# Performance work log

Hardware: AMD Instinct MI355X
Metric: run time of the kernel (lower is better)

Reference implementation:

```python
import jax, jax.numpy as jnp
import numpy as np

EPS = 1e-8  # torch.nn.CosineSimilarity default eps


def setup_inputs() -> dict:
    key = jax.random.key(0)
    k1, k2 = jax.random.split(key)
    action_set = jax.random.normal(k1, (1_000_000, 64), dtype=jnp.float32)
    pred_action = jax.random.normal(k2, (32, 4, 64), dtype=jnp.float32)
    return {"pred_action": pred_action, "action_set": action_set}


def reference(pred_action, action_set):
    # pred_action: [B, T, D] (a 2-D [B, D] input would be unsqueezed to T=1)
    # action_set:  [N, D]
    if pred_action.ndim == 2:
        pred_action = pred_action[:, None, :]
    # torch CosineSimilarity: x1.x2 / max(||x1|| * ||x2||, eps)
    dot = jnp.einsum('nd,btd->nbt', action_set, pred_action)        # [N, B, T]
    na = jnp.linalg.norm(action_set, axis=-1)                       # [N]
    nb = jnp.linalg.norm(pred_action, axis=-1)                      # [B, T]
    sims = dot / jnp.maximum(na[:, None, None] * nb[None, :, :], EPS)
    amax = jnp.argmax(sims, axis=0)                                  # [B, T]
    return action_set[amax]                                          # [B, T, D]
```

## Files before the change

kernel.cpp:

```cpp
#include <hip/hip_runtime.h>
#include <hip/hip_bf16.h>
#include <math.h>

#define D        64
#define NQ       128
#define TS       64
#define ASTRIDE  72
#define MARGIN   0.025f
#define CAP      128

typedef __attribute__((ext_vector_type(8))) short  short8;
typedef __attribute__((ext_vector_type(4))) short  short4v;
typedef __attribute__((ext_vector_type(4))) float  f32x4;

__device__ inline unsigned ordf(float f) {
    unsigned u = __float_as_uint(f);
    return (u & 0x80000000u) ? ~u : (u | 0x80000000u);
}

__device__ inline short bf16bits(float f) {
    __hip_bfloat16 h = __float2bfloat16(f);
    return *(short*)&h;
}

__device__ inline float sq4(f32x4 a) {
    float s = 0.f;
    s = fmaf(a.x, a.x, s); s = fmaf(a.y, a.y, s);
    s = fmaf(a.z, a.z, s); s = fmaf(a.w, a.w, s);
    return s;
}

__device__ inline float sq16(f32x4 a, f32x4 b, f32x4 c, f32x4 d) {
    return sq4(a) + sq4(b) + sq4(c) + sq4(d);
}

__device__ inline short8 cvt8(f32x4 a, f32x4 b, float s) {
    short8 r;
    r[0] = bf16bits(a.x * s); r[1] = bf16bits(a.y * s);
    r[2] = bf16bits(a.z * s); r[3] = bf16bits(a.w * s);
    r[4] = bf16bits(b.x * s); r[5] = bf16bits(b.y * s);
    r[6] = bf16bits(b.z * s); r[7] = bf16bits(b.w * s);
    return r;
}

__device__ inline short4v cvt4(f32x4 a, float s) {
    short4v r;
    r[0] = bf16bits(a.x * s); r[1] = bf16bits(a.y * s);
    r[2] = bf16bits(a.z * s); r[3] = bf16bits(a.w * s);
    return r;
}

__global__ __launch_bounds__(256, 3)
void k1_score(const float* __restrict__ pred,
              const float* __restrict__ acts,
              float* __restrict__ tmax,
              int ntiles)
{
    __shared__ unsigned short As[2][TS * ASTRIDE];

    const int tid  = threadIdx.x;
    const int lane = tid & 63;
    const int wv   = tid >> 6;
    const int quad = lane >> 4;
    const int l15  = lane & 15;

    short8 bf[2][2];
#pragma unroll
    for (int nt = 0; nt < 2; ++nt) {
        const int q = (wv * 2 + nt) * 16 + l15;
        const float* P = pred + q * D + quad * 8;
        f32x4 v0 = *(const f32x4*)(P);
        f32x4 v1 = *(const f32x4*)(P + 4);
        f32x4 v2 = *(const f32x4*)(P + 32);
        f32x4 v3 = *(const f32x4*)(P + 36);
        float nb2 = sq16(v0, v1, v2, v3);
        nb2 += __shfl_xor(nb2, 16);
        nb2 += __shfl_xor(nb2, 32);
        const float rnb = 1.0f / sqrtf(nb2);
        bf[nt][0] = cvt8(v0, v1, rnb);
        bf[nt][1] = cvt8(v2, v3, rnb);
    }

    int tile = blockIdx.x;
    if (tile >= ntiles) return;

    {
        const f32x4* src = (const f32x4*)(acts + (size_t)tile * (TS * D));
        f32x4 v[4];
#pragma unroll
        for (int i = 0; i < 4; ++i) v[i] = src[tid + i * 256];
#pragma unroll
        for (int i = 0; i < 4; ++i) {
            const int c   = tid + i * 256;
            const int row = c >> 4, col = c & 15;
            float s = sq4(v[i]);
            s += __shfl_xor(s, 1); s += __shfl_xor(s, 2);
            s += __shfl_xor(s, 4); s += __shfl_xor(s, 8);
            *(short4v*)&As[0][row * ASTRIDE + col * 4] = cvt4(v[i], 1.0f / sqrtf(s));
        }
    }
    __syncthreads();

    int p = 0;
    while (true) {
        const int tn = tile + gridDim.x;
        const bool have_next = tn < ntiles;

        f32x4 v[4];
        if (have_next) {
            const f32x4* src = (const f32x4*)(acts + (size_t)tn * (TS * D));
#pragma unroll
            for (int i = 0; i < 4; ++i) v[i] = src[tid + i * 256];
        }

        short8 af[4][2];
#pragma unroll
        for (int mt = 0; mt < 4; ++mt)
#pragma unroll
            for (int ks = 0; ks < 2; ++ks)
                af[mt][ks] = *(const short8*)
                    &As[p][(mt * 16 + l15) * ASTRIDE + ks * 32 + quad * 8];

        f32x4 acc[2][4];
#pragma unroll
        for (int nt = 0; nt < 2; ++nt)
#pragma unroll
            for (int mt = 0; mt < 4; ++mt) acc[nt][mt] = (f32x4){0.f, 0.f, 0.f, 0.f};
#pragma unroll
        for (int ks = 0; ks < 2; ++ks)
#pragma unroll
            for (int nt = 0; nt < 2; ++nt)
#pragma unroll
                for (int mt = 0; mt < 4; ++mt)
                    acc[nt][mt] = __builtin_amdgcn_mfma_f32_16x16x32_bf16(
                        af[mt][ks], bf[nt][ks], acc[nt][mt], 0, 0, 0);

#pragma unroll
        for (int nt = 0; nt < 2; ++nt) {
            float m = -3.0e38f;
#pragma unroll
            for (int mt = 0; mt < 4; ++mt)
                m = fmaxf(m, fmaxf(fmaxf(acc[nt][mt].x, acc[nt][mt].y),
                                   fmaxf(acc[nt][mt].z, acc[nt][mt].w)));
            m = fmaxf(m, __shfl_xor(m, 16));
            m = fmaxf(m, __shfl_xor(m, 32));
            if (quad == 0) {
                const int q = (wv * 2 + nt) * 16 + l15;
                tmax[(size_t)q * ntiles + tile] = m;
            }
        }

        if (!have_next) break;

#pragma unroll
        for (int i = 0; i < 4; ++i) {
            const int c   = tid + i * 256;
            const int row = c >> 4, col = c & 15;
            float s = sq4(v[i]);
            s += __shfl_xor(s, 1); s += __shfl_xor(s, 2);
            s += __shfl_xor(s, 4); s += __shfl_xor(s, 8);
            *(short4v*)&As[p ^ 1][row * ASTRIDE + col * 4] = cvt4(v[i], 1.0f / sqrtf(s));
        }
        __syncthreads();
        p ^= 1;
        tile = tn;
    }
}

__global__ __launch_bounds__(256, 2)
void k2_rescore(const float* __restrict__ pred,
                const float* __restrict__ acts,
                const float* __restrict__ tmax,
                float* __restrict__ out,
                int ntiles)
{
    __shared__ float wmax[4];
    __shared__ int   cnt;
    __shared__ int   list[CAP];

    const int q   = blockIdx.x;
    const int tid = threadIdx.x;
    const float* row = tmax + (size_t)q * ntiles;

    if (tid == 0) cnt = 0;
    float m = -3.0e38f;
    for (int t = tid; t < ntiles; t += 256) m = fmaxf(m, row[t]);
#pragma unroll
    for (int off = 1; off < 64; off <<= 1) m = fmaxf(m, __shfl_xor(m, off));
    if ((tid & 63) == 0) wmax[tid >> 6] = m;
    __syncthreads();
    m = fmaxf(fmaxf(wmax[0], wmax[1]), fmaxf(wmax[2], wmax[3]));
    const float thr = m - MARGIN;

    for (int t = tid; t < ntiles; t += 256) {
        if (row[t] >= thr) {
            int i = atomicAdd(&cnt, 1);
            if (i < CAP) list[i] = t;
        }
    }
    __syncthreads();
    const int n = min(cnt, CAP);

    if (tid < 64) {
        const f32x4* P = (const f32x4*)(pred + q * D);
        unsigned long long best = 0ull;
        for (int i = 0; i < n; ++i) {
            const int r = list[i] * TS + tid;
            const f32x4* A = (const f32x4*)(acts + (size_t)r * D);
            float dot = 0.f, na2 = 0.f;
#pragma unroll
            for (int c = 0; c < 16; ++c) {
                f32x4 a = A[c];
                f32x4 pq = P[c];
                dot = fmaf(a.x, pq.x, dot); na2 = fmaf(a.x, a.x, na2);
                dot = fmaf(a.y, pq.y, dot); na2 = fmaf(a.y, a.y, na2);
                dot = fmaf(a.z, pq.z, dot); na2 = fmaf(a.z, a.z, na2);
                dot = fmaf(a.w, pq.w, dot); na2 = fmaf(a.w, a.w, na2);
            }
            float sim = dot * (1.0f / sqrtf(na2));
            unsigned long long key =
                ((unsigned long long)ordf(sim) << 32) | (unsigned)(~r);
#pragma unroll
            for (int off = 1; off < 64; off <<= 1) {
                unsigned long long o = __shfl_xor(key, off);
                if (o > key) key = o;
            }
            if (key > best) best = key;
        }
        const unsigned idx = ~(unsigned)(best & 0xffffffffull);
        out[q * D + tid] = acts[(size_t)idx * D + tid];
    }
}

extern "C" void kernel_launch(void* const* d_in, const int* in_sizes, int n_in,
                              void* d_out, int out_size, void* d_ws, size_t ws_size,
                              hipStream_t stream)
{
    const float* pred = (const float*)d_in[0];
    const float* acts = (const float*)d_in[1];
    long n0 = in_sizes[0], n1 = in_sizes[1];
    if (n0 > n1) {
        const float* t = pred; pred = acts; acts = t;
        long tt = n0; n0 = n1; n1 = tt;
    }
    const int N      = (int)(n1 / D);
    const int ntiles = N / TS;

    float* tmax = (float*)d_ws;
    float* out  = (float*)d_out;

    k1_score<<<dim3(768), dim3(256), 0, stream>>>(pred, acts, tmax, ntiles);
    k2_rescore<<<dim3(NQ), dim3(256), 0, stream>>>(pred, acts, tmax, out, ntiles);
}
```

Measured before the change: 382.4 us.

## Assign contiguous tile chunks per block and coalesce tmax writes via LDS

Each block of the scoring kernel now processes a contiguous chunk of 21 tiles instead of grid-strided tiles. Per-tile maxima are buffered in shared memory and written to tmax in row-contiguous runs at the end, replacing the scattered per-tile stores. The rescoring kernel spreads candidate tiles across all four waves and reduces the best key once at the end, instead of running one wave with a shuffle reduction per candidate. The extra shared buffer lowers occupancy headroom, and the grid size now depends on ntiles.

```diff
diff --git a/kernel.cpp b/kernel.cpp
--- a/kernel.cpp
+++ b/kernel.cpp
@@ -8,6 +8,7 @@
 #define ASTRIDE  72
 #define MARGIN   0.025f
 #define CAP      128
+#define CHUNK    21
 
 typedef __attribute__((ext_vector_type(8))) short  short8;
 typedef __attribute__((ext_vector_type(4))) short  short4v;
@@ -57,12 +58,17 @@
               int ntiles)
 {
     __shared__ unsigned short As[2][TS * ASTRIDE];
+    __shared__ float tbuf[NQ * CHUNK];
 
     const int tid  = threadIdx.x;
     const int lane = tid & 63;
     const int wv   = tid >> 6;
     const int quad = lane >> 4;
     const int l15  = lane & 15;
+
+    const int tile0 = blockIdx.x * CHUNK;
+    if (tile0 >= ntiles) return;
+    const int cn = min(CHUNK, ntiles - tile0);
 
     short8 bf[2][2];
 #pragma unroll
@@ -81,11 +87,8 @@
         bf[nt][1] = cvt8(v2, v3, rnb);
     }
 
-    int tile = blockIdx.x;
-    if (tile >= ntiles) return;
-
     {
-        const f32x4* src = (const f32x4*)(acts + (size_t)tile * (TS * D));
+        const f32x4* src = (const f32x4*)(acts + (size_t)tile0 * (TS * D));
         f32x4 v[4];
 #pragma unroll
         for (int i = 0; i < 4; ++i) v[i] = src[tid + i * 256];
@@ -101,14 +104,15 @@
     }
     __syncthreads();
 
-    int p = 0;
+    int ti = 0;
+    int p  = 0;
     while (true) {
-        const int tn = tile + gridDim.x;
-        const bool have_next = tn < ntiles;
+        const bool have_next = (ti + 1) < cn;
 
         f32x4 v[4];
         if (have_next) {
-            const f32x4* src = (const f32x4*)(acts + (size_t)tn * (TS * D));
+            const f32x4* src =
+                (const f32x4*)(acts + (size_t)(tile0 + ti + 1) * (TS * D));
 #pragma unroll
             for (int i = 0; i < 4; ++i) v[i] = src[tid + i * 256];
         }
@@ -146,7 +150,7 @@
             m = fmaxf(m, __shfl_xor(m, 32));
             if (quad == 0) {
                 const int q = (wv * 2 + nt) * 16 + l15;
-                tmax[(size_t)q * ntiles + tile] = m;
+                tbuf[q * CHUNK + ti] = m;
             }
         }
 
@@ -163,7 +167,14 @@
         }
         __syncthreads();
         p ^= 1;
-        tile = tn;
+        ++ti;
+    }
+
+    __syncthreads();
+    for (int idx = tid; idx < NQ * CHUNK; idx += 256) {
+        const int q = idx / CHUNK;
+        const int t = idx - q * CHUNK;
+        if (t < cn) tmax[(size_t)q * ntiles + tile0 + t] = tbuf[idx];
     }
 }
 
@@ -177,9 +188,12 @@
     __shared__ float wmax[4];
     __shared__ int   cnt;
     __shared__ int   list[CAP];
-
-    const int q   = blockIdx.x;
-    const int tid = threadIdx.x;
+    __shared__ unsigned long long wbest[4];
+
+    const int q    = blockIdx.x;
+    const int tid  = threadIdx.x;
+    const int lane = tid & 63;
+    const int wv   = tid >> 6;
     const float* row = tmax + (size_t)q * ntiles;
 
     if (tid == 0) cnt = 0;
@@ -187,7 +201,7 @@
     for (int t = tid; t < ntiles; t += 256) m = fmaxf(m, row[t]);
 #pragma unroll
     for (int off = 1; off < 64; off <<= 1) m = fmaxf(m, __shfl_xor(m, off));
-    if ((tid & 63) == 0) wmax[tid >> 6] = m;
+    if (lane == 0) wmax[wv] = m;
     __syncthreads();
     m = fmaxf(fmaxf(wmax[0], wmax[1]), fmaxf(wmax[2], wmax[3]));
     const float thr = m - MARGIN;
@@ -201,33 +215,42 @@
     __syncthreads();
     const int n = min(cnt, CAP);
 
+    const f32x4* P = (const f32x4*)(pred + q * D);
+    unsigned long long best = 0ull;
+    for (int i = wv; i < n; i += 4) {
+        const int r = list[i] * TS + lane;
+        const f32x4* A = (const f32x4*)(acts + (size_t)r * D);
+        float dot = 0.f, na2 = 0.f;
+#pragma unroll
+        for (int c = 0; c < 16; ++c) {
+            f32x4 a  = A[c];
+            f32x4 pq = P[c];
+            dot = fmaf(a.x, pq.x, dot); na2 = fmaf(a.x, a.x, na2);
+            dot = fmaf(a.y, pq.y, dot); na2 = fmaf(a.y, a.y, na2);
+            dot = fmaf(a.z, pq.z, dot); na2 = fmaf(a.z, a.z, na2);
+            dot = fmaf(a.w, pq.w, dot); na2 = fmaf(a.w, a.w, na2);
+        }
+        float sim = dot * (1.0f / sqrtf(na2));
+        unsigned long long key =
+            ((unsigned long long)ordf(sim) << 32) | (unsigned)(~r);
+        if (key > best) best = key;
+    }
+#pragma unroll
+    for (int off = 1; off < 64; off <<= 1) {
+        unsigned long long o = __shfl_xor(best, off);
+        if (o > best) best = o;
+    }
+    if (lane == 0) wbest[wv] = best;
+    __syncthreads();
+    if (tid == 0) {
+        unsigned long long b = wbest[0];
+#pragma unroll
+        for (int w = 1; w < 4; ++w) if (wbest[w] > b) b = wbest[w];
+        wbest[0] = b;
+    }
+    __syncthreads();
     if (tid < 64) {
-        const f32x4* P = (const f32x4*)(pred + q * D);
-        unsigned long long best = 0ull;
-        for (int i = 0; i < n; ++i) {
-            const int r = list[i] * TS + tid;
-            const f32x4* A = (const f32x4*)(acts + (size_t)r * D);
-            float dot = 0.f, na2 = 0.f;
-#pragma unroll
-            for (int c = 0; c < 16; ++c) {
-                f32x4 a = A[c];
-                f32x4 pq = P[c];
-                dot = fmaf(a.x, pq.x, dot); na2 = fmaf(a.x, a.x, na2);
-                dot = fmaf(a.y, pq.y, dot); na2 = fmaf(a.y, a.y, na2);
-                dot = fmaf(a.z, pq.z, dot); na2 = fmaf(a.z, a.z, na2);
-                dot = fmaf(a.w, pq.w, dot); na2 = fmaf(a.w, a.w, na2);
-            }
-            float sim = dot * (1.0f / sqrtf(na2));
-            unsigned long long key =
-                ((unsigned long long)ordf(sim) << 32) | (unsigned)(~r);
-#pragma unroll
-            for (int off = 1; off < 64; off <<= 1) {
-                unsigned long long o = __shfl_xor(key, off);
-                if (o > key) key = o;
-            }
-            if (key > best) best = key;
-        }
-        const unsigned idx = ~(unsigned)(best & 0xffffffffull);
+        const unsigned idx = ~(unsigned)(wbest[0] & 0xffffffffull);
         out[q * D + tid] = acts[(size_t)idx * D + tid];
     }
 }
@@ -245,10 +268,11 @@
     }
     const int N      = (int)(n1 / D);
     const int ntiles = N / TS;
+    const int nblk   = (ntiles + CHUNK - 1) / CHUNK;
 
     float* tmax = (float*)d_ws;
     float* out  = (float*)d_out;
 
-    k1_score<<<dim3(768), dim3(256), 0, stream>>>(pred, acts, tmax, ntiles);
+    k1_score<<<dim3(nblk), dim3(256), 0, stream>>>(pred, acts, tmax, ntiles);
     k2_rescore<<<dim3(NQ), dim3(256), 0, stream>>>(pred, acts, tmax, out, ntiles);
 }
```

Result: no change. 382.6 us (+0.1%).
